# Kernel optimization log

Measured on AMD Instinct MI355X. Metric: run time of the kernel, lower is better.

Reference implementation:

```python
import jax, jax.numpy as jnp
import numpy as np

B, T, C = 2, 2048, 2048
H, KV = 16, 4
D = C // H            # 128 head dim
G = H // KV           # 4 query heads per kv head
THETA = 10000.0


def setup_inputs() -> dict:
    key = jax.random.key(0)
    k0, k1, k2, k3 = jax.random.split(key, 4)
    s = 1.0 / np.sqrt(C)
    return {
        "x": jax.random.normal(k0, (B, T, C), jnp.float32),
        "Wq": jax.random.normal(k1, (H * D, C), jnp.float32) * s,
        "Wkv": jax.random.normal(k2, (2 * KV * D, C), jnp.float32) * s,
        "Wo": jax.random.normal(k3, (C, C), jnp.float32) * s,
    }


def _rotate_half(x):
    d = x.shape[-1] // 2
    return jnp.concatenate([-x[..., d:], x[..., :d]], axis=-1)


def _rope_tables(t, d):
    freqs = 1.0 / (THETA ** (jnp.arange(0, d, 2, dtype=jnp.float32) / d))
    ang = jnp.arange(t, dtype=jnp.float32)[:, None] * freqs[None, :]  # [T, d/2]
    emb = jnp.concatenate([ang, ang], axis=-1)                         # [T, d]
    return jnp.cos(emb), jnp.sin(emb)


def reference(x, Wq, Wkv, Wo):
    b, t, c = x.shape
    q = (x @ Wq.T).reshape(b, t, H, D).transpose(0, 2, 1, 3)      # [B,H,T,D]
    kv = (x @ Wkv.T).reshape(b, t, 2 * KV, D)
    k = kv[:, :, :KV].transpose(0, 2, 1, 3)                        # [B,KV,T,D]
    v = kv[:, :, KV:].transpose(0, 2, 1, 3)                        # [B,KV,T,D]

    cos, sin = _rope_tables(t, D)
    cos, sin = cos[None, None], sin[None, None]                    # [1,1,T,D]
    q = q * cos + _rotate_half(q) * sin
    k = k * cos + _rotate_half(k) * sin

    # GQA: keep k/v at KV heads; reshape q into [B,KV,G,T,D] instead of expanding k/v.
    qg = q.reshape(b, KV, G, t, D)
    scores = jnp.einsum('bkgtd,bksd->bkgts', qg, k) / jnp.sqrt(jnp.float32(D))
    causal = jnp.tril(jnp.ones((t, t), dtype=bool))                # is_causal=True path
    scores = jnp.where(causal, scores, -jnp.inf)
    p = jax.nn.softmax(scores, axis=-1)
    y = jnp.einsum('bkgts,bksd->bkgtd', p, v)                      # [B,KV,G,T,D]
    y = y.reshape(b, H, t, D).transpose(0, 2, 1, 3).reshape(b, t, c)
    return y @ Wo.T
```

## Files before the change

### kernel.cpp

```cpp
#include <hip/hip_runtime.h>

typedef unsigned short u16;
typedef __attribute__((ext_vector_type(4))) float f32x4;
typedef __attribute__((ext_vector_type(8))) __bf16 bf16x8;

__device__ __forceinline__ u16 f2bf(float f) {
    unsigned int x = __float_as_uint(f);
    x += 0x7fffu + ((x >> 16) & 1u);
    return (u16)(x >> 16);
}
__device__ __forceinline__ float bf2f(u16 u) {
    return __uint_as_float(((unsigned int)u) << 16);
}
__device__ __forceinline__ void async16(const void* g, void* l) {
    __builtin_amdgcn_global_load_lds(
        (const __attribute__((address_space(1))) void*)g,
        (__attribute__((address_space(3))) void*)l,
        16, 0, 0);
}
__device__ __forceinline__ void barrier_fence() {
    asm volatile("" ::: "memory");
    __builtin_amdgcn_s_barrier();
    asm volatile("" ::: "memory");
}

__global__ __launch_bounds__(256)
void cvt_all(const float* __restrict__ x,  const float* __restrict__ wq,
             const float* __restrict__ wkv, const float* __restrict__ wo,
             u16* __restrict__ xb, u16* __restrict__ wqb,
             u16* __restrict__ wkvb, u16* __restrict__ wob)
{
    const int nx = 8388608, nq = 4194304, nkv = 2097152;
    const int i = (blockIdx.x * 256 + threadIdx.x) * 4;
    const float* src; u16* dst; int off;
    if (i < nx)                 { src = x;   dst = xb;   off = i; }
    else if (i < nx + nq)       { src = wq;  dst = wqb;  off = i - nx; }
    else if (i < nx + nq + nkv) { src = wkv; dst = wkvb; off = i - nx - nq; }
    else                        { src = wo;  dst = wob;  off = i - nx - nq - nkv; }
    const float4 v = *(const float4*)(src + off);
    ushort4 o;
    o.x = f2bf(v.x); o.y = f2bf(v.y); o.z = f2bf(v.z); o.w = f2bf(v.w);
    *(ushort4*)(dst + off) = o;
}

template <int MODE>
__global__ __launch_bounds__(256, 3)
void gemm128r(const u16* __restrict__ A,
              const u16* __restrict__ B0,
              const u16* __restrict__ B1,
              u16* __restrict__ C,
              float* __restrict__ Cf,
              u16* __restrict__ vbuf,
              int M, int N, int K)
{
    constexpr int ASZ = 128 * 32;
    __shared__ __align__(16) u16 As[3 * ASZ];
    __shared__ __align__(16) u16 Bs[3 * ASZ];

    const int tid  = threadIdx.x;
    const int w    = tid >> 6;
    const int lane = tid & 63;
    const int fl   = lane & 15;
    const int q4   = lane >> 4;
    const int wm   = w >> 1;
    const int wn   = w & 1;

    const int gx  = gridDim.x;
    const int nwg = gx * gridDim.y;
    int id = blockIdx.y * gx + blockIdx.x;
    id = (id & 7) * (nwg >> 3) + (id >> 3);
    const int m0 = (id / gx) * 128;
    const int n0 = (id % gx) * 128;

    const u16* Bp = B0;
    int nb = n0;
    if (MODE == 1 && n0 >= 2048) { Bp = B1; nb = n0 - 2048; }

    const int srow = w * 16 + (lane >> 2);
    const int sg   = (lane & 3) ^ ((lane >> 3) & 3);
    const u16* agp = A  + (size_t)(m0 + srow) * K + sg * 8;
    const u16* bgp = Bp + (size_t)(nb + srow) * K + sg * 8;
    const int sLds = w * 512;

    const int cSlot = (q4 ^ ((fl >> 1) & 3)) * 8;

    f32x4 acc[4][4];
    #pragma unroll
    for (int i = 0; i < 4; ++i)
        #pragma unroll
        for (int j = 0; j < 4; ++j)
            acc[i][j] = f32x4{0.f, 0.f, 0.f, 0.f};

    const int NT = K >> 5;

    auto stage = [&](int t, int bf) {
        const size_t kof = (size_t)t * 32;
        async16(agp + kof,                   &As[bf * ASZ + sLds]);
        async16(agp + (size_t)64 * K + kof,  &As[bf * ASZ + 2048 + sLds]);
        async16(bgp + kof,                   &Bs[bf * ASZ + sLds]);
        async16(bgp + (size_t)64 * K + kof,  &Bs[bf * ASZ + 2048 + sLds]);
    };

    stage(0, 0);
    stage(1, 1);

    int bf = 0;
    for (int t = 0; t < NT; ++t) {
        if (t < NT - 1) asm volatile("s_waitcnt vmcnt(4)" ::: "memory");
        else            asm volatile("s_waitcnt vmcnt(0)" ::: "memory");
        barrier_fence();
        const int bf2 = (bf + 2 >= 3) ? bf - 1 : bf + 2;
        if (t + 2 < NT) stage(t + 2, bf2);

        const int ab = bf * ASZ + (wm * 64 + fl) * 32 + cSlot;
        const int bb = bf * ASZ + (wn * 64 + fl) * 32 + cSlot;
        bf16x8 a[4], b[4];
        #pragma unroll
        for (int mt = 0; mt < 4; ++mt)
            a[mt] = *(const bf16x8*)&As[ab + mt * 512];
        #pragma unroll
        for (int nt = 0; nt < 4; ++nt)
            b[nt] = *(const bf16x8*)&Bs[bb + nt * 512];

        #pragma unroll
        for (int mt = 0; mt < 4; ++mt)
            #pragma unroll
            for (int nt = 0; nt < 4; ++nt)
                acc[mt][nt] = __builtin_amdgcn_mfma_f32_16x16x32_bf16(
                    a[mt], b[nt], acc[mt][nt], 0, 0, 0);

        bf = (bf + 1 >= 3) ? 0 : bf + 1;
    }

    #pragma unroll
    for (int mt = 0; mt < 4; ++mt) {
        #pragma unroll
        for (int nt = 0; nt < 4; ++nt) {
            const int colb = n0 + wn * 64 + nt * 16 + fl;
            #pragma unroll
            for (int r = 0; r < 4; ++r) {
                const int row = m0 + wm * 64 + mt * 16 + q4 * 4 + r;
                if (MODE == 0) {
                    Cf[(size_t)row * N + colb] = acc[mt][nt][r];
                } else {
                    const u16 val = f2bf(acc[mt][nt][r]);
                    if (colb < 2560) {
                        C[(size_t)row * 3072 + colb] = val;
                    } else {
                        const int f  = colb - 2560;
                        const int tt = row & 2047;
                        const int bb2 = row >> 11;
                        vbuf[((size_t)((bb2 << 2) + (f >> 7)) * 128 + (f & 127)) * 2048 + tt] = val;
                    }
                }
            }
        }
    }
}

__global__ __launch_bounds__(256)
void rope_kernel(u16* __restrict__ qkv)
{
    const int idx = blockIdx.x * 256 + threadIdx.x;
    const int i   = idx & 63;
    const int t1  = idx >> 6;
    const int hh  = t1 % 20;
    const int m   = t1 / 20;
    const int pos = m & 2047;
    const bool isq = (hh < 16);
    const int col = isq ? (hh << 7) : (2048 + ((hh - 16) << 7));
    u16* p = qkv + (size_t)m * 3072 + col;

    const float inv = powf(10000.0f, -(float)(2 * i) * (1.0f / 128.0f));
    const float ang = (float)pos * inv;
    float s, c;
    sincosf(ang, &s, &c);
    const float sc = isq ? 0.08838834764831845f : 1.0f;
    const float x1 = bf2f(p[i]);
    const float x2 = bf2f(p[i + 64]);
    p[i]      = f2bf((x1 * c - x2 * s) * sc);
    p[i + 64] = f2bf((x2 * c + x1 * s) * sc);
}

__global__ __launch_bounds__(256, 2)
void attn_kernel(const u16* __restrict__ qkv,
                 const u16* __restrict__ vsrc,
                 u16* __restrict__ y)
{
    constexpr int T = 2048;
    const int lo  = blockIdx.x;
    const int hi  = 31 - lo;
    const int bh  = blockIdx.y;
    const int b   = bh >> 4;
    const int h   = bh & 15;
    const int kvh = h >> 2;

    const int tid  = threadIdx.x;
    const int w    = tid >> 6;
    const int lane = tid & 63;
    const int fl   = lane & 15;
    const int q4   = lane >> 4;

    __shared__ __align__(16) u16 Ks[2][64 * 128];
    __shared__ __align__(16) u16 Vt[2][128 * 64];
    __shared__ __align__(16) u16 Ps[64 * 72];

    const u16* Qg = qkv  + (size_t)(b * T) * 3072 + (h << 7);
    const u16* Kg = qkv  + (size_t)(b * T) * 3072 + 2048 + (kvh << 7);
    const u16* Vg = vsrc + (size_t)((b * 4 + kvh) * 128) * T;

    bf16x8 qf0[4], qf1[4];
    #pragma unroll
    for (int kc = 0; kc < 4; ++kc) {
        qf0[kc] = *(const bf16x8*)&Qg[(size_t)(lo * 64 + w * 16 + fl) * 3072 + kc * 32 + q4 * 8];
        qf1[kc] = *(const bf16x8*)&Qg[(size_t)(hi * 64 + w * 16 + fl) * 3072 + kc * 32 + q4 * 8];
    }

    int goffK[4], goffV[4], ldsC[4];
    #pragma unroll
    for (int i = 0; i < 4; ++i) {
        const int c  = w + 4 * i;
        const int rk = 4 * c + (lane >> 4);
        const int lk = (lane & 15) ^ (rk & 15);
        goffK[i] = rk * 3072 + lk * 8;
        const int rv = 8 * c + (lane >> 3);
        const int lv = (lane & 7) ^ ((lane >> 3) & 7);
        goffV[i] = rv * T + lv * 8;
        ldsC[i]  = c * 512;
    }

    #pragma unroll
    for (int i = 0; i < 4; ++i) {
        async16(Kg + goffK[i], &Ks[0][ldsC[i]]);
        async16(Vg + goffV[i], &Vt[0][ldsC[i]]);
    }

    float l0 = 0.f, l1 = 0.f;
    f32x4 o0[8], o1[8];
    #pragma unroll
    for (int dt = 0; dt < 8; ++dt) {
        o0[dt] = f32x4{0.f, 0.f, 0.f, 0.f};
        o1[dt] = f32x4{0.f, 0.f, 0.f, 0.f};
    }

    const int psrow = (w * 16 + fl) * 72;

    for (int j = 0; j <= hi; ++j) {
        __syncthreads();

        if (j < hi) {
            const u16* kb = Kg + (size_t)(j + 1) * 64 * 3072;
            const u16* vb = Vg + (j + 1) * 64;
            const int nb = (j + 1) & 1;
            #pragma unroll
            for (int i = 0; i < 4; ++i) {
                async16(kb + goffK[i], &Ks[nb][ldsC[i]]);
                async16(vb + goffV[i], &Vt[nb][ldsC[i]]);
            }
        }
        const int cb = j & 1;
        const bool dual = (j <= lo);

        f32x4 s0[4], s1[4];
        #pragma unroll
        for (int nt = 0; nt < 4; ++nt) {
            s0[nt] = f32x4{0.f, 0.f, 0.f, 0.f};
            s1[nt] = f32x4{0.f, 0.f, 0.f, 0.f};
        }
        if (dual) {
            #pragma unroll
            for (int kc = 0; kc < 4; ++kc)
                #pragma unroll
                for (int nt = 0; nt < 4; ++nt) {
                    bf16x8 aK = *(const bf16x8*)
                        &Ks[cb][(nt * 16 + fl) * 128 + (((kc << 2) + q4) ^ fl) * 8];
                    s1[nt] = __builtin_amdgcn_mfma_f32_16x16x32_bf16(aK, qf1[kc], s1[nt], 0, 0, 0);
                    s0[nt] = __builtin_amdgcn_mfma_f32_16x16x32_bf16(aK, qf0[kc], s0[nt], 0, 0, 0);
                }
        } else {
            #pragma unroll
            for (int kc = 0; kc < 4; ++kc)
                #pragma unroll
                for (int nt = 0; nt < 4; ++nt) {
                    bf16x8 aK = *(const bf16x8*)
                        &Ks[cb][(nt * 16 + fl) * 128 + (((kc << 2) + q4) ^ fl) * 8];
                    s1[nt] = __builtin_amdgcn_mfma_f32_16x16x32_bf16(aK, qf1[kc], s1[nt], 0, 0, 0);
                }
        }

        if (j == lo || j == hi) {
            const int qloc = w * 16 + fl;
            #pragma unroll
            for (int nt = 0; nt < 4; ++nt)
                #pragma unroll
                for (int r = 0; r < 4; ++r)
                    if (nt * 16 + q4 * 4 + r > qloc) {
                        if (j == lo) s0[nt][r] = -3e38f;
                        else         s1[nt][r] = -3e38f;
                    }
        }

        if (dual) {
            #pragma unroll
            for (int nt = 0; nt < 4; ++nt) {
                ushort4 pw;
                float p0 = __expf(s0[nt][0]);
                float p1 = __expf(s0[nt][1]);
                float p2 = __expf(s0[nt][2]);
                float p3 = __expf(s0[nt][3]);
                l0 += (p0 + p1) + (p2 + p3);
                pw.x = f2bf(p0); pw.y = f2bf(p1); pw.z = f2bf(p2); pw.w = f2bf(p3);
                *(ushort4*)&Ps[psrow + nt * 16 + q4 * 4] = pw;
            }
            asm volatile("s_waitcnt lgkmcnt(0)" ::: "memory");
            #pragma unroll
            for (int kc = 0; kc < 2; ++kc) {
                bf16x8 ap = *(const bf16x8*)&Ps[psrow + kc * 32 + q4 * 8];
                #pragma unroll
                for (int dt = 0; dt < 8; ++dt) {
                    bf16x8 bv = *(const bf16x8*)
                        &Vt[cb][(dt * 16 + fl) * 64 + (((kc << 2) + q4) ^ (fl & 7)) * 8];
                    o0[dt] = __builtin_amdgcn_mfma_f32_16x16x32_bf16(ap, bv, o0[dt], 0, 0, 0);
                }
            }
        }

        #pragma unroll
        for (int nt = 0; nt < 4; ++nt) {
            ushort4 pw;
            float p0 = __expf(s1[nt][0]);
            float p1 = __expf(s1[nt][1]);
            float p2 = __expf(s1[nt][2]);
            float p3 = __expf(s1[nt][3]);
            l1 += (p0 + p1) + (p2 + p3);
            pw.x = f2bf(p0); pw.y = f2bf(p1); pw.z = f2bf(p2); pw.w = f2bf(p3);
            *(ushort4*)&Ps[psrow + nt * 16 + q4 * 4] = pw;
        }
        asm volatile("s_waitcnt lgkmcnt(0)" ::: "memory");
        #pragma unroll
        for (int kc = 0; kc < 2; ++kc) {
            bf16x8 ap = *(const bf16x8*)&Ps[psrow + kc * 32 + q4 * 8];
            #pragma unroll
            for (int dt = 0; dt < 8; ++dt) {
                bf16x8 bv = *(const bf16x8*)
                    &Vt[cb][(dt * 16 + fl) * 64 + (((kc << 2) + q4) ^ (fl & 7)) * 8];
                o1[dt] = __builtin_amdgcn_mfma_f32_16x16x32_bf16(ap, bv, o1[dt], 0, 0, 0);
            }
        }
    }

    l0 += __shfl_xor(l0, 16, 64);
    l0 += __shfl_xor(l0, 32, 64);
    l1 += __shfl_xor(l1, 16, 64);
    l1 += __shfl_xor(l1, 32, 64);
    const float li0 = 1.0f / l0;
    const float li1 = 1.0f / l1;

    float lr0[4], lr1[4];
    #pragma unroll
    for (int r = 0; r < 4; ++r) {
        lr0[r] = __shfl(li0, q4 * 4 + r, 16);
        lr1[r] = __shfl(li1, q4 * 4 + r, 16);
    }
    #pragma unroll
    for (int dt = 0; dt < 8; ++dt)
        #pragma unroll
        for (int r = 0; r < 4; ++r) {
            const int row0 = lo * 64 + w * 16 + q4 * 4 + r;
            const int row1 = hi * 64 + w * 16 + q4 * 4 + r;
            y[(size_t)(b * T + row0) * 2048 + (h << 7) + dt * 16 + fl] =
                f2bf(o0[dt][r] * lr0[r]);
            y[(size_t)(b * T + row1) * 2048 + (h << 7) + dt * 16 + fl] =
                f2bf(o1[dt][r] * lr1[r]);
        }
}

extern "C" void kernel_launch(void* const* d_in, const int* in_sizes, int n_in,
                              void* d_out, int out_size, void* d_ws, size_t ws_size,
                              hipStream_t stream)
{
    const float* x   = (const float*)d_in[0];
    const float* Wq  = (const float*)d_in[1];
    const float* Wkv = (const float*)d_in[2];
    const float* Wo  = (const float*)d_in[3];
    float* out = (float*)d_out;

    const int nx = 4096 * 2048, nq = 2048 * 2048, nkv = 1024 * 2048, no = 2048 * 2048;

    u16* xb   = (u16*)d_ws;
    u16* wqb  = xb  + nx;
    u16* wkvb = wqb + nq;
    u16* wob  = wkvb + nkv;
    u16* qkv  = wob + no;
    u16* vbuf = qkv + (size_t)4096 * 3072;
    u16* y    = vbuf + (size_t)2 * 4 * 128 * 2048;

    const int ntot = nx + nq + nkv + no;
    cvt_all<<<ntot / 1024, 256, 0, stream>>>(x, Wq, Wkv, Wo, xb, wqb, wkvb, wob);

    dim3 g1(3072 / 128, 4096 / 128);
    gemm128r<1><<<g1, 256, 0, stream>>>(xb, wqb, wkvb, qkv, nullptr, vbuf, 4096, 3072, 2048);

    rope_kernel<<<(4096 * 20 * 64) / 256, 256, 0, stream>>>(qkv);

    attn_kernel<<<dim3(16, 32), 256, 0, stream>>>(qkv, vbuf, y);

    dim3 g2(2048 / 128, 4096 / 128);
    gemm128r<0><<<g2, 256, 0, stream>>>(y, wob, nullptr, nullptr, out, nullptr, 4096, 2048, 2048);
}
```

Measured before the change: 309.9 us.

## Load K/V fragments directly from global in attention; add 64-row output GEMM

The attention kernel stops staging K and V tiles through double-buffered shared memory. Each wave now reads its MFMA operand fragments straight from global memory, which removes the per-tile __syncthreads and most of the LDS footprint. P for both query tiles is written to a widened Ps buffer so the PV MFMAs for the two tiles share each V fragment load. The output projection switches to a new 64x128-tile GEMM with a triple-buffered async pipeline and workgroup-order swizzling, giving more blocks and higher occupancy. The risk is that the global K/V reads are less coalesced, are repeated across waves and rely on cache, and sit on the critical path with no prefetch.

```diff
diff --git a/kernel.cpp b/kernel.cpp
--- a/kernel.cpp
+++ b/kernel.cpp
@@ -158,6 +158,100 @@
     }
 }
 
+__global__ __launch_bounds__(256, 4)
+void gemm64(const u16* __restrict__ A,
+            const u16* __restrict__ B0,
+            float* __restrict__ Cf,
+            int M, int N, int K)
+{
+    constexpr int ASZ = 64 * 32;
+    constexpr int BSZ = 128 * 32;
+    __shared__ __align__(16) u16 As[3 * ASZ];
+    __shared__ __align__(16) u16 Bs[3 * BSZ];
+
+    const int tid  = threadIdx.x;
+    const int w    = tid >> 6;
+    const int lane = tid & 63;
+    const int fl   = lane & 15;
+    const int q4   = lane >> 4;
+    const int wm   = w >> 1;
+    const int wn   = w & 1;
+
+    const int gx  = gridDim.x;
+    const int nwg = gx * gridDim.y;
+    int id = blockIdx.y * gx + blockIdx.x;
+    id = (id & 7) * (nwg >> 3) + (id >> 3);
+    const int m0 = (id / gx) * 64;
+    const int n0 = (id % gx) * 128;
+
+    const int srow = w * 16 + (lane >> 2);
+    const int sg   = (lane & 3) ^ ((lane >> 3) & 3);
+    const u16* agp = A  + (size_t)(m0 + srow) * K + sg * 8;
+    const u16* bgp = B0 + (size_t)(n0 + srow) * K + sg * 8;
+    const int sLds = w * 512;
+
+    const int cSlot = (q4 ^ ((fl >> 1) & 3)) * 8;
+
+    f32x4 acc[2][4];
+    #pragma unroll
+    for (int i = 0; i < 2; ++i)
+        #pragma unroll
+        for (int j = 0; j < 4; ++j)
+            acc[i][j] = f32x4{0.f, 0.f, 0.f, 0.f};
+
+    const int NT = K >> 5;
+
+    auto stage = [&](int t, int bf) {
+        const size_t kof = (size_t)t * 32;
+        async16(agp + kof,                  &As[bf * ASZ + sLds]);
+        async16(bgp + kof,                  &Bs[bf * BSZ + sLds]);
+        async16(bgp + (size_t)64 * K + kof, &Bs[bf * BSZ + 2048 + sLds]);
+    };
+
+    stage(0, 0);
+    stage(1, 1);
+
+    int bf = 0;
+    for (int t = 0; t < NT; ++t) {
+        if (t < NT - 1) asm volatile("s_waitcnt vmcnt(3)" ::: "memory");
+        else            asm volatile("s_waitcnt vmcnt(0)" ::: "memory");
+        barrier_fence();
+        const int bf2 = (bf + 2 >= 3) ? bf - 1 : bf + 2;
+        if (t + 2 < NT) stage(t + 2, bf2);
+
+        const int ab = bf * ASZ + (wm * 32 + fl) * 32 + cSlot;
+        const int bb = bf * BSZ + (wn * 64 + fl) * 32 + cSlot;
+        bf16x8 a[2], b[4];
+        #pragma unroll
+        for (int mt = 0; mt < 2; ++mt)
+            a[mt] = *(const bf16x8*)&As[ab + mt * 512];
+        #pragma unroll
+        for (int nt = 0; nt < 4; ++nt)
+            b[nt] = *(const bf16x8*)&Bs[bb + nt * 512];
+
+        #pragma unroll
+        for (int mt = 0; mt < 2; ++mt)
+            #pragma unroll
+            for (int nt = 0; nt < 4; ++nt)
+                acc[mt][nt] = __builtin_amdgcn_mfma_f32_16x16x32_bf16(
+                    a[mt], b[nt], acc[mt][nt], 0, 0, 0);
+
+        bf = (bf + 1 >= 3) ? 0 : bf + 1;
+    }
+
+    #pragma unroll
+    for (int mt = 0; mt < 2; ++mt)
+        #pragma unroll
+        for (int nt = 0; nt < 4; ++nt) {
+            const int colb = n0 + wn * 64 + nt * 16 + fl;
+            #pragma unroll
+            for (int r = 0; r < 4; ++r) {
+                const int row = m0 + wm * 32 + mt * 16 + q4 * 4 + r;
+                Cf[(size_t)row * N + colb] = acc[mt][nt][r];
+            }
+        }
+}
+
 __global__ __launch_bounds__(256)
 void rope_kernel(u16* __restrict__ qkv)
 {
@@ -201,9 +295,7 @@
     const int fl   = lane & 15;
     const int q4   = lane >> 4;
 
-    __shared__ __align__(16) u16 Ks[2][64 * 128];
-    __shared__ __align__(16) u16 Vt[2][128 * 64];
-    __shared__ __align__(16) u16 Ps[64 * 72];
+    __shared__ __align__(16) u16 Ps[64 * 136];
 
     const u16* Qg = qkv  + (size_t)(b * T) * 3072 + (h << 7);
     const u16* Kg = qkv  + (size_t)(b * T) * 3072 + 2048 + (kvh << 7);
@@ -216,24 +308,14 @@
         qf1[kc] = *(const bf16x8*)&Qg[(size_t)(hi * 64 + w * 16 + fl) * 3072 + kc * 32 + q4 * 8];
     }
 
-    int goffK[4], goffV[4], ldsC[4];
-    #pragma unroll
-    for (int i = 0; i < 4; ++i) {
-        const int c  = w + 4 * i;
-        const int rk = 4 * c + (lane >> 4);
-        const int lk = (lane & 15) ^ (rk & 15);
-        goffK[i] = rk * 3072 + lk * 8;
-        const int rv = 8 * c + (lane >> 3);
-        const int lv = (lane & 7) ^ ((lane >> 3) & 7);
-        goffV[i] = rv * T + lv * 8;
-        ldsC[i]  = c * 512;
-    }
-
-    #pragma unroll
-    for (int i = 0; i < 4; ++i) {
-        async16(Kg + goffK[i], &Ks[0][ldsC[i]]);
-        async16(Vg + goffV[i], &Vt[0][ldsC[i]]);
-    }
+    const u16* kr[4];
+    #pragma unroll
+    for (int nt = 0; nt < 4; ++nt)
+        kr[nt] = Kg + (size_t)(nt * 16 + fl) * 3072 + q4 * 8;
+    const u16* vr[8];
+    #pragma unroll
+    for (int dt = 0; dt < 8; ++dt)
+        vr[dt] = Vg + (size_t)(dt * 16 + fl) * T + q4 * 8;
 
     float l0 = 0.f, l1 = 0.f;
     f32x4 o0[8], o1[8];
@@ -243,23 +325,12 @@
         o1[dt] = f32x4{0.f, 0.f, 0.f, 0.f};
     }
 
-    const int psrow = (w * 16 + fl) * 72;
+    const int psrow = (w * 16 + fl) * 136;
 
     for (int j = 0; j <= hi; ++j) {
-        __syncthreads();
-
-        if (j < hi) {
-            const u16* kb = Kg + (size_t)(j + 1) * 64 * 3072;
-            const u16* vb = Vg + (j + 1) * 64;
-            const int nb = (j + 1) & 1;
-            #pragma unroll
-            for (int i = 0; i < 4; ++i) {
-                async16(kb + goffK[i], &Ks[nb][ldsC[i]]);
-                async16(vb + goffV[i], &Vt[nb][ldsC[i]]);
-            }
-        }
-        const int cb = j & 1;
         const bool dual = (j <= lo);
+        const size_t kjo = (size_t)j * 64 * 3072;
+        const int    vjo = j * 64;
 
         f32x4 s0[4], s1[4];
         #pragma unroll
@@ -272,8 +343,7 @@
             for (int kc = 0; kc < 4; ++kc)
                 #pragma unroll
                 for (int nt = 0; nt < 4; ++nt) {
-                    bf16x8 aK = *(const bf16x8*)
-                        &Ks[cb][(nt * 16 + fl) * 128 + (((kc << 2) + q4) ^ fl) * 8];
+                    bf16x8 aK = *(const bf16x8*)(kr[nt] + kjo + kc * 32);
                     s1[nt] = __builtin_amdgcn_mfma_f32_16x16x32_bf16(aK, qf1[kc], s1[nt], 0, 0, 0);
                     s0[nt] = __builtin_amdgcn_mfma_f32_16x16x32_bf16(aK, qf0[kc], s0[nt], 0, 0, 0);
                 }
@@ -282,8 +352,7 @@
             for (int kc = 0; kc < 4; ++kc)
                 #pragma unroll
                 for (int nt = 0; nt < 4; ++nt) {
-                    bf16x8 aK = *(const bf16x8*)
-                        &Ks[cb][(nt * 16 + fl) * 128 + (((kc << 2) + q4) ^ fl) * 8];
+                    bf16x8 aK = *(const bf16x8*)(kr[nt] + kjo + kc * 32);
                     s1[nt] = __builtin_amdgcn_mfma_f32_16x16x32_bf16(aK, qf1[kc], s1[nt], 0, 0, 0);
                 }
         }
@@ -310,21 +379,9 @@
                 float p3 = __expf(s0[nt][3]);
                 l0 += (p0 + p1) + (p2 + p3);
                 pw.x = f2bf(p0); pw.y = f2bf(p1); pw.z = f2bf(p2); pw.w = f2bf(p3);
-                *(ushort4*)&Ps[psrow + nt * 16 + q4 * 4] = pw;
+                *(ushort4*)&Ps[psrow + 64 + nt * 16 + q4 * 4] = pw;
             }
-            asm volatile("s_waitcnt lgkmcnt(0)" ::: "memory");
-            #pragma unroll
-            for (int kc = 0; kc < 2; ++kc) {
-                bf16x8 ap = *(const bf16x8*)&Ps[psrow + kc * 32 + q4 * 8];
-                #pragma unroll
-                for (int dt = 0; dt < 8; ++dt) {
-                    bf16x8 bv = *(const bf16x8*)
-                        &Vt[cb][(dt * 16 + fl) * 64 + (((kc << 2) + q4) ^ (fl & 7)) * 8];
-                    o0[dt] = __builtin_amdgcn_mfma_f32_16x16x32_bf16(ap, bv, o0[dt], 0, 0, 0);
-                }
-            }
-        }
-
+        }
         #pragma unroll
         for (int nt = 0; nt < 4; ++nt) {
             ushort4 pw;
@@ -337,14 +394,28 @@
             *(ushort4*)&Ps[psrow + nt * 16 + q4 * 4] = pw;
         }
         asm volatile("s_waitcnt lgkmcnt(0)" ::: "memory");
-        #pragma unroll
-        for (int kc = 0; kc < 2; ++kc) {
-            bf16x8 ap = *(const bf16x8*)&Ps[psrow + kc * 32 + q4 * 8];
-            #pragma unroll
-            for (int dt = 0; dt < 8; ++dt) {
-                bf16x8 bv = *(const bf16x8*)
-                    &Vt[cb][(dt * 16 + fl) * 64 + (((kc << 2) + q4) ^ (fl & 7)) * 8];
-                o1[dt] = __builtin_amdgcn_mfma_f32_16x16x32_bf16(ap, bv, o1[dt], 0, 0, 0);
+
+        if (dual) {
+            #pragma unroll
+            for (int kc = 0; kc < 2; ++kc) {
+                bf16x8 ap1 = *(const bf16x8*)&Ps[psrow + kc * 32 + q4 * 8];
+                bf16x8 ap0 = *(const bf16x8*)&Ps[psrow + 64 + kc * 32 + q4 * 8];
+                #pragma unroll
+                for (int dt = 0; dt < 8; ++dt) {
+                    bf16x8 bv = *(const bf16x8*)(vr[dt] + vjo + kc * 32);
+                    o1[dt] = __builtin_amdgcn_mfma_f32_16x16x32_bf16(ap1, bv, o1[dt], 0, 0, 0);
+                    o0[dt] = __builtin_amdgcn_mfma_f32_16x16x32_bf16(ap0, bv, o0[dt], 0, 0, 0);
+                }
+            }
+        } else {
+            #pragma unroll
+            for (int kc = 0; kc < 2; ++kc) {
+                bf16x8 ap1 = *(const bf16x8*)&Ps[psrow + kc * 32 + q4 * 8];
+                #pragma unroll
+                for (int dt = 0; dt < 8; ++dt) {
+                    bf16x8 bv = *(const bf16x8*)(vr[dt] + vjo + kc * 32);
+                    o1[dt] = __builtin_amdgcn_mfma_f32_16x16x32_bf16(ap1, bv, o1[dt], 0, 0, 0);
+                }
             }
         }
     }
@@ -405,6 +476,6 @@
 
     attn_kernel<<<dim3(16, 32), 256, 0, stream>>>(qkv, vbuf, y);
 
-    dim3 g2(2048 / 128, 4096 / 128);
-    gemm128r<0><<<g2, 256, 0, stream>>>(y, wob, nullptr, nullptr, out, nullptr, 4096, 2048, 2048);
-}
+    dim3 g2(2048 / 128, 4096 / 64);
+    gemm64<<<g2, 256, 0, stream>>>(y, wob, out, 4096, 2048, 2048);
+}
```

After: 485.1 us. 56.5% more time.

## Fuse RoPE and query scaling into QKV GEMM epilogue, drop rope kernel

Applied to the files above, without the earlier changes.

Reassigns warp column tiles in the QKV GEMM so that each warp holds both halves (i and i+64) of a head's rotary pair. The RoPE rotation and the 1/sqrt(D) query scaling can then be applied in registers before the bf16 store. This removes the separate rope kernel launch along with its read-modify-write pass over the Q/K buffer. The cost is fast-math __sincosf and exp2f with a hardcoded constant, which may lose accuracy at large positions, plus extra epilogue work inside the GEMM.

```diff
diff --git a/kernel.cpp b/kernel.cpp
--- a/kernel.cpp
+++ b/kernel.cpp
@@ -43,15 +43,13 @@
     *(ushort4*)(dst + off) = o;
 }
 
-template <int MODE>
 __global__ __launch_bounds__(256, 3)
-void gemm128r(const u16* __restrict__ A,
+void gemm_qkv(const u16* __restrict__ A,
               const u16* __restrict__ B0,
               const u16* __restrict__ B1,
               u16* __restrict__ C,
-              float* __restrict__ Cf,
               u16* __restrict__ vbuf,
-              int M, int N, int K)
+              int M, int K)
 {
     constexpr int ASZ = 128 * 32;
     __shared__ __align__(16) u16 As[3 * ASZ];
@@ -74,7 +72,7 @@
 
     const u16* Bp = B0;
     int nb = n0;
-    if (MODE == 1 && n0 >= 2048) { Bp = B1; nb = n0 - 2048; }
+    if (n0 >= 2048) { Bp = B1; nb = n0 - 2048; }
 
     const int srow = w * 16 + (lane >> 2);
     const int sg   = (lane & 3) ^ ((lane >> 3) & 3);
@@ -113,14 +111,15 @@
         if (t + 2 < NT) stage(t + 2, bf2);
 
         const int ab = bf * ASZ + (wm * 64 + fl) * 32 + cSlot;
-        const int bb = bf * ASZ + (wn * 64 + fl) * 32 + cSlot;
+        const int bb = bf * ASZ + (wn * 32 + fl) * 32 + cSlot;
         bf16x8 a[4], b[4];
         #pragma unroll
         for (int mt = 0; mt < 4; ++mt)
             a[mt] = *(const bf16x8*)&As[ab + mt * 512];
-        #pragma unroll
-        for (int nt = 0; nt < 4; ++nt)
-            b[nt] = *(const bf16x8*)&Bs[bb + nt * 512];
+        b[0] = *(const bf16x8*)&Bs[bb];
+        b[1] = *(const bf16x8*)&Bs[bb + 512];
+        b[2] = *(const bf16x8*)&Bs[bb + 2048];
+        b[3] = *(const bf16x8*)&Bs[bb + 2560];
 
         #pragma unroll
         for (int mt = 0; mt < 4; ++mt)
@@ -132,54 +131,141 @@
         bf = (bf + 1 >= 3) ? 0 : bf + 1;
     }
 
-    #pragma unroll
-    for (int mt = 0; mt < 4; ++mt) {
+    if (n0 < 2560) {
+        const float sc = (n0 < 2048) ? 0.08838834764831845f : 1.0f;
+        float inv[2];
+        #pragma unroll
+        for (int j = 0; j < 2; ++j)
+            inv[j] = exp2f(-(float)(wn * 32 + j * 16 + fl) * 0.2076205f);
+        #pragma unroll
+        for (int mt = 0; mt < 4; ++mt) {
+            #pragma unroll
+            for (int r = 0; r < 4; ++r) {
+                const int row = m0 + wm * 64 + mt * 16 + q4 * 4 + r;
+                const float pos = (float)(row & 2047);
+                #pragma unroll
+                for (int j = 0; j < 2; ++j) {
+                    float s, c;
+                    __sincosf(pos * inv[j], &s, &c);
+                    const float x1 = acc[mt][j][r];
+                    const float x2 = acc[mt][j + 2][r];
+                    const int i0 = wn * 32 + j * 16 + fl;
+                    C[(size_t)row * 3072 + n0 + i0]      = f2bf((x1 * c - x2 * s) * sc);
+                    C[(size_t)row * 3072 + n0 + 64 + i0] = f2bf((x2 * c + x1 * s) * sc);
+                }
+            }
+        }
+    } else {
+        #pragma unroll
+        for (int mt = 0; mt < 4; ++mt)
+            #pragma unroll
+            for (int j = 0; j < 4; ++j) {
+                const int colb = n0 + wn * 32 + (j & 1) * 16 + (j >> 1) * 64 + fl;
+                const int f = colb - 2560;
+                #pragma unroll
+                for (int r = 0; r < 4; ++r) {
+                    const int row = m0 + wm * 64 + mt * 16 + q4 * 4 + r;
+                    const int tt = row & 2047;
+                    const int bb2 = row >> 11;
+                    vbuf[((size_t)((bb2 << 2) + (f >> 7)) * 128 + (f & 127)) * 2048 + tt] =
+                        f2bf(acc[mt][j][r]);
+                }
+            }
+    }
+}
+
+__global__ __launch_bounds__(256, 3)
+void gemm128r(const u16* __restrict__ A,
+              const u16* __restrict__ B0,
+              float* __restrict__ Cf,
+              int M, int N, int K)
+{
+    constexpr int ASZ = 128 * 32;
+    __shared__ __align__(16) u16 As[3 * ASZ];
+    __shared__ __align__(16) u16 Bs[3 * ASZ];
+
+    const int tid  = threadIdx.x;
+    const int w    = tid >> 6;
+    const int lane = tid & 63;
+    const int fl   = lane & 15;
+    const int q4   = lane >> 4;
+    const int wm   = w >> 1;
+    const int wn   = w & 1;
+
+    const int gx  = gridDim.x;
+    const int nwg = gx * gridDim.y;
+    int id = blockIdx.y * gx + blockIdx.x;
+    id = (id & 7) * (nwg >> 3) + (id >> 3);
+    const int m0 = (id / gx) * 128;
+    const int n0 = (id % gx) * 128;
+
+    const int srow = w * 16 + (lane >> 2);
+    const int sg   = (lane & 3) ^ ((lane >> 3) & 3);
+    const u16* agp = A  + (size_t)(m0 + srow) * K + sg * 8;
+    const u16* bgp = B0 + (size_t)(n0 + srow) * K + sg * 8;
+    const int sLds = w * 512;
+
+    const int cSlot = (q4 ^ ((fl >> 1) & 3)) * 8;
+
+    f32x4 acc[4][4];
+    #pragma unroll
+    for (int i = 0; i < 4; ++i)
+        #pragma unroll
+        for (int j = 0; j < 4; ++j)
+            acc[i][j] = f32x4{0.f, 0.f, 0.f, 0.f};
+
+    const int NT = K >> 5;
+
+    auto stage = [&](int t, int bf) {
+        const size_t kof = (size_t)t * 32;
+        async16(agp + kof,                   &As[bf * ASZ + sLds]);
+        async16(agp + (size_t)64 * K + kof,  &As[bf * ASZ + 2048 + sLds]);
+        async16(bgp + kof,                   &Bs[bf * ASZ + sLds]);
+        async16(bgp + (size_t)64 * K + kof,  &Bs[bf * ASZ + 2048 + sLds]);
+    };
+
+    stage(0, 0);
+    stage(1, 1);
+
+    int bf = 0;
+    for (int t = 0; t < NT; ++t) {
+        if (t < NT - 1) asm volatile("s_waitcnt vmcnt(4)" ::: "memory");
+        else            asm volatile("s_waitcnt vmcnt(0)" ::: "memory");
+        barrier_fence();
+        const int bf2 = (bf + 2 >= 3) ? bf - 1 : bf + 2;
+        if (t + 2 < NT) stage(t + 2, bf2);
+
+        const int ab = bf * ASZ + (wm * 64 + fl) * 32 + cSlot;
+        const int bb = bf * ASZ + (wn * 64 + fl) * 32 + cSlot;
+        bf16x8 a[4], b[4];
+        #pragma unroll
+        for (int mt = 0; mt < 4; ++mt)
+            a[mt] = *(const bf16x8*)&As[ab + mt * 512];
+        #pragma unroll
+        for (int nt = 0; nt < 4; ++nt)
+            b[nt] = *(const bf16x8*)&Bs[bb + nt * 512];
+
+        #pragma unroll
+        for (int mt = 0; mt < 4; ++mt)
+            #pragma unroll
+            for (int nt = 0; nt < 4; ++nt)
+                acc[mt][nt] = __builtin_amdgcn_mfma_f32_16x16x32_bf16(
+                    a[mt], b[nt], acc[mt][nt], 0, 0, 0);
+
+        bf = (bf + 1 >= 3) ? 0 : bf + 1;
+    }
+
+    #pragma unroll
+    for (int mt = 0; mt < 4; ++mt)
         #pragma unroll
         for (int nt = 0; nt < 4; ++nt) {
             const int colb = n0 + wn * 64 + nt * 16 + fl;
             #pragma unroll
             for (int r = 0; r < 4; ++r) {
                 const int row = m0 + wm * 64 + mt * 16 + q4 * 4 + r;
-                if (MODE == 0) {
-                    Cf[(size_t)row * N + colb] = acc[mt][nt][r];
-                } else {
-                    const u16 val = f2bf(acc[mt][nt][r]);
-                    if (colb < 2560) {
-                        C[(size_t)row * 3072 + colb] = val;
-                    } else {
-                        const int f  = colb - 2560;
-                        const int tt = row & 2047;
-                        const int bb2 = row >> 11;
-                        vbuf[((size_t)((bb2 << 2) + (f >> 7)) * 128 + (f & 127)) * 2048 + tt] = val;
-                    }
-                }
-            }
-        }
-    }
-}
-
-__global__ __launch_bounds__(256)
-void rope_kernel(u16* __restrict__ qkv)
-{
-    const int idx = blockIdx.x * 256 + threadIdx.x;
-    const int i   = idx & 63;
-    const int t1  = idx >> 6;
-    const int hh  = t1 % 20;
-    const int m   = t1 / 20;
-    const int pos = m & 2047;
-    const bool isq = (hh < 16);
-    const int col = isq ? (hh << 7) : (2048 + ((hh - 16) << 7));
-    u16* p = qkv + (size_t)m * 3072 + col;
-
-    const float inv = powf(10000.0f, -(float)(2 * i) * (1.0f / 128.0f));
-    const float ang = (float)pos * inv;
-    float s, c;
-    sincosf(ang, &s, &c);
-    const float sc = isq ? 0.08838834764831845f : 1.0f;
-    const float x1 = bf2f(p[i]);
-    const float x2 = bf2f(p[i + 64]);
-    p[i]      = f2bf((x1 * c - x2 * s) * sc);
-    p[i + 64] = f2bf((x2 * c + x1 * s) * sc);
+                Cf[(size_t)row * N + colb] = acc[mt][nt][r];
+            }
+        }
 }
 
 __global__ __launch_bounds__(256, 2)
@@ -399,12 +485,10 @@
     cvt_all<<<ntot / 1024, 256, 0, stream>>>(x, Wq, Wkv, Wo, xb, wqb, wkvb, wob);
 
     dim3 g1(3072 / 128, 4096 / 128);
-    gemm128r<1><<<g1, 256, 0, stream>>>(xb, wqb, wkvb, qkv, nullptr, vbuf, 4096, 3072, 2048);
-
-    rope_kernel<<<(4096 * 20 * 64) / 256, 256, 0, stream>>>(qkv);
+    gemm_qkv<<<g1, 256, 0, stream>>>(xb, wqb, wkvb, qkv, vbuf, 4096, 2048);
 
     attn_kernel<<<dim3(16, 32), 256, 0, stream>>>(qkv, vbuf, y);
 
     dim3 g2(2048 / 128, 4096 / 128);
-    gemm128r<0><<<g2, 256, 0, stream>>>(y, wob, nullptr, nullptr, out, nullptr, 4096, 2048, 2048);
-}
+    gemm128r<<<g2, 256, 0, stream>>>(y, wob, out, 4096, 2048, 2048);
+}
```

New measurement: 273.3 us. 11.8% less time.
